# Kernel tuning notes

Hardware: AMD Instinct MI355X
Metric: run time of the kernel (lower is better)

The kernel has to match this reference:

```python
import jax, jax.numpy as jnp
import numpy as np

N_HEAD = 16
D_MODEL = 1024
D_K = 64
D_V = 64
LN_EPS = 1e-6


def setup_inputs() -> dict:
    key = jax.random.key(0)
    ks = jax.random.split(key, 10)
    B, S = 2, 2048
    scale = 0.02
    return {
        "q": jax.random.normal(ks[0], (B, S, D_MODEL), jnp.float32),
        "k": jax.random.normal(ks[1], (B, S, D_MODEL), jnp.float32),
        "v": jax.random.normal(ks[2], (B, S, D_MODEL), jnp.float32),
        "Wq": jax.random.normal(ks[3], (D_MODEL, N_HEAD * D_K), jnp.float32) * scale,
        "Wk": jax.random.normal(ks[4], (D_MODEL, N_HEAD * D_K), jnp.float32) * scale,
        "Wv": jax.random.normal(ks[5], (D_MODEL, N_HEAD * D_V), jnp.float32) * scale,
        "Wfc": jax.random.normal(ks[6], (N_HEAD * D_V, D_MODEL), jnp.float32) * scale,
        "bfc": jnp.zeros((D_MODEL,), jnp.float32),
        "gamma": jnp.ones((D_MODEL,), jnp.float32),
        "beta": jnp.zeros((D_MODEL,), jnp.float32),
    }


def reference(q, k, v, Wq, Wk, Wv, Wfc, bfc, gamma, beta):
    B, S, _ = q.shape
    residual = q
    # QKV projections, split into heads: [B, S, H, Dh]
    qh = (q @ Wq).reshape(B, S, N_HEAD, D_K)
    kh = (k @ Wk).reshape(B, S, N_HEAD, D_K)
    vh = (v @ Wv).reshape(B, S, N_HEAD, D_V)
    # scaled dot-product attention (explicit score matrix, as in source)
    temperature = jnp.asarray(D_K, qh.dtype) ** 0.5
    attn = jnp.einsum("bqhd,bkhd->bhqk", qh, kh) / temperature
    attn = jax.nn.softmax(attn, axis=-1)
    out = jnp.einsum("bhqk,bkhd->bqhd", attn, vh).reshape(B, S, N_HEAD * D_V)
    # output projection (dropout is identity in eval mode)
    out = out @ Wfc + bfc
    # residual + layernorm (eps=1e-6)
    x = out + residual
    mu = jnp.mean(x, axis=-1, keepdims=True)
    var = jnp.mean(jnp.square(x - mu), axis=-1, keepdims=True)
    return (x - mu) / jnp.sqrt(var + LN_EPS) * gamma + beta
```

## Files before the change

kernel.cpp:

```cpp
#include <hip/hip_runtime.h>

typedef float f32x4 __attribute__((ext_vector_type(4)));
typedef short short8 __attribute__((ext_vector_type(8)));
typedef short short4v __attribute__((ext_vector_type(4)));
typedef unsigned short ushort_t;

#define D_MODEL 1024
#define N_HEAD 16
#define SEQ 2048
#define BATCH 2
#define M_TOK 4096
#define HD 1024
#define NT 32
#define APANEL 131072
#define WPANEL 32768
#define QSCALE_L2E 0.1803368801111f

__device__ __forceinline__ ushort_t f2bf(float f) {
    union { float f; unsigned int u; } x; x.f = f;
    unsigned int r = x.u + 0x7fffu + ((x.u >> 16) & 1u);
    return (ushort_t)(r >> 16);
}
__device__ __forceinline__ ushort_t f2bf_fast(float f) {
    union { float f; unsigned int u; } x; x.f = f;
    return (ushort_t)((x.u + 0x8000u) >> 16);
}

__device__ __forceinline__ void async_copy16(const ushort_t* gptr, ushort_t* lptr) {
    __builtin_amdgcn_global_load_lds(
        (const __attribute__((address_space(1))) unsigned int*)gptr,
        (__attribute__((address_space(3))) unsigned int*)lptr, 16, 0, 0);
}

__global__ __launch_bounds__(256) void prep_fused(const float* __restrict__ w0,
                                                  const float* __restrict__ w1,
                                                  const float* __restrict__ w2,
                                                  const float* __restrict__ w3,
                                                  ushort_t* __restrict__ o0,
                                                  ushort_t* __restrict__ o1,
                                                  ushort_t* __restrict__ o2,
                                                  ushort_t* __restrict__ o3,
                                                  const float* __restrict__ q,
                                                  const float* __restrict__ k,
                                                  const float* __restrict__ v,
                                                  ushort_t* __restrict__ qo,
                                                  ushort_t* __restrict__ ko,
                                                  ushort_t* __restrict__ vo) {
    const int z = blockIdx.z;
    const int tid = threadIdx.x;
    const int flat = blockIdx.x + 64 * blockIdx.y;
    if (z < 4) {
        if (flat >= 1024) return;
        const int C = D_MODEL;
        const float* in = (z == 0) ? w0 : (z == 1) ? w1 : (z == 2) ? w2 : w3;
        ushort_t* out = (z == 0) ? o0 : (z == 1) ? o1 : (z == 2) ? o2 : o3;
        __shared__ ushort_t t[32][33];
        int bc = (flat & 31) * 32, br = (flat >> 5) * 32;
        int tx = tid & 31, ty = tid >> 5;
        for (int i = ty; i < 32; i += 8)
            t[i][tx] = f2bf(in[(size_t)(br + i) * C + bc + tx]);
        __syncthreads();
        size_t pbase = (size_t)(br >> 5) * WPANEL;
        for (int i = ty; i < 32; i += 8)
            out[pbase + (size_t)(bc + i) * 32 + tx] = t[tx][i];
    } else {
        const float* s = (z == 4) ? q : (z == 5) ? k : v;
        ushort_t* d = (z == 4) ? qo : (z == 5) ? ko : vo;
        size_t i = ((size_t)flat * 256 + tid) * 8;
        int m = (int)(i >> 10), k0 = (int)(i & 1023);
        float4 a = *(const float4*)(s + i);
        float4 b = *(const float4*)(s + i + 4);
        ushort_t tmp[8] = {f2bf(a.x), f2bf(a.y), f2bf(a.z), f2bf(a.w),
                           f2bf(b.x), f2bf(b.y), f2bf(b.z), f2bf(b.w)};
        *(short8*)(d + (size_t)(k0 >> 5) * APANEL + (size_t)m * 32 + (k0 & 31)) = *(short8*)tmp;
    }
}

__global__ __launch_bounds__(256) void gemm_qkv(const ushort_t* __restrict__ qb,
                                                const ushort_t* __restrict__ kb,
                                                const ushort_t* __restrict__ vb,
                                                const ushort_t* __restrict__ wq,
                                                const ushort_t* __restrict__ wk,
                                                const ushort_t* __restrict__ wv,
                                                ushort_t* __restrict__ Qo,
                                                ushort_t* __restrict__ Ko,
                                                ushort_t* __restrict__ V4) {
    __shared__ ushort_t As[2][128 * 32];
    __shared__ ushort_t Bs[2][128 * 32];
    const int z = blockIdx.z;
    const ushort_t* A = (z == 0) ? qb : (z == 1) ? kb : vb;
    const ushort_t* Bt = (z == 0) ? wq : (z == 1) ? wk : wv;
    const int tid = threadIdx.x;
    const int wave = tid >> 6, lane = tid & 63;
    const int quad = lane >> 4, l16 = lane & 15;
    const int m0 = blockIdx.y * 128, n0 = blockIdx.x * 128;
    const int wm = (wave >> 1) * 64, wn = (wave & 1) * 64;
    const int N = D_MODEL;

    f32x4 acc[4][4];
    for (int i = 0; i < 4; ++i)
        for (int j = 0; j < 4; ++j) acc[i][j] = (f32x4){0.f, 0.f, 0.f, 0.f};

    for (int it = 0; it < 16; ++it) {
        __syncthreads();
        const ushort_t* Ap = A + (size_t)(it * 2) * APANEL + (size_t)m0 * 32;
        const ushort_t* Bp = Bt + (size_t)(it * 2) * WPANEL + (size_t)n0 * 32;
        #pragma unroll
        for (int hf = 0; hf < 2; ++hf) {
            #pragma unroll
            for (int c = 0; c < 2; ++c) {
                int off = (wave * 2 + c) * 512;
                async_copy16(Ap + hf * APANEL + off + lane * 8, &As[hf][off] + lane * 8);
                async_copy16(Bp + hf * WPANEL + off + lane * 8, &Bs[hf][off] + lane * 8);
            }
        }
        __syncthreads();
        short8 af[4][2], bfr[4][2];
        #pragma unroll
        for (int i = 0; i < 4; ++i)
            #pragma unroll
            for (int sk = 0; sk < 2; ++sk)
                af[i][sk] = *(const short8*)&As[sk][(wm + i * 16 + l16) * 32 + quad * 8];
        #pragma unroll
        for (int j = 0; j < 4; ++j)
            #pragma unroll
            for (int sk = 0; sk < 2; ++sk)
                bfr[j][sk] = *(const short8*)&Bs[sk][(wn + j * 16 + l16) * 32 + quad * 8];
        #pragma unroll
        for (int sk = 0; sk < 2; ++sk)
            #pragma unroll
            for (int i = 0; i < 4; ++i)
                #pragma unroll
                for (int j = 0; j < 4; ++j)
                    acc[i][j] = __builtin_amdgcn_mfma_f32_16x16x32_bf16(af[i][sk], bfr[j][sk], acc[i][j], 0, 0, 0);
    }
    if (z == 2) {
        const int tile64 = m0 + wm;
        const int b2 = tile64 >> 11;
        const int kt = (tile64 & 2047) >> 6;
        #pragma unroll
        for (int i = 0; i < 4; ++i)
            #pragma unroll
            for (int j = 0; j < 4; ++j) {
                int n = n0 + wn + j * 16 + l16;
                int h2 = n >> 6, d = n & 63;
                int quadR = (quad + ((n >> 2) & 3)) & 3;
                ushort_t tmp[4];
                #pragma unroll
                for (int r = 0; r < 4; ++r) tmp[r] = f2bf(acc[i][j][r]);
                size_t dst = ((((size_t)(h2 * 2 + b2) * NT + kt) * 4 + i) << 10) + d * 16 + quadR * 4;
                *(short4v*)&V4[dst] = *(short4v*)tmp;
            }
    } else {
        ushort_t* C = (z == 0) ? Qo : Ko;
        const float scale = (z == 0) ? QSCALE_L2E : 1.0f;
        #pragma unroll
        for (int i = 0; i < 4; ++i)
            #pragma unroll
            for (int j = 0; j < 4; ++j) {
                int n = n0 + wn + j * 16 + l16;
                #pragma unroll
                for (int r = 0; r < 4; ++r) {
                    int m = m0 + wm + i * 16 + quad * 4 + r;
                    C[(size_t)m * N + n] = f2bf(acc[i][j][r] * scale);
                }
            }
    }
}

__global__ __launch_bounds__(256) void gemm_fc(const ushort_t* __restrict__ A,
                                               const ushort_t* __restrict__ Bt,
                                               float* __restrict__ Cf,
                                               const float* __restrict__ bias,
                                               const float* __restrict__ resid) {
    __shared__ ushort_t As[2][128 * 32];
    __shared__ ushort_t Bs[2][64 * 32];
    const int tid = threadIdx.x;
    const int wave = tid >> 6, lane = tid & 63;
    const int quad = lane >> 4, l16 = lane & 15;
    const int m0 = blockIdx.y * 128, n0 = blockIdx.x * 64;
    const int N = D_MODEL;

    f32x4 acc[2][4];
    for (int i = 0; i < 2; ++i)
        for (int j = 0; j < 4; ++j) acc[i][j] = (f32x4){0.f, 0.f, 0.f, 0.f};

    for (int it = 0; it < 16; ++it) {
        __syncthreads();
        const ushort_t* Ap = A + (size_t)(it * 2) * APANEL + (size_t)m0 * 32;
        const ushort_t* Bp = Bt + (size_t)(it * 2) * WPANEL + (size_t)n0 * 32;
        #pragma unroll
        for (int c = 0; c < 4; ++c) {
            int g = wave * 4 + c;
            int sk = g >> 3, off = (g & 7) * 512;
            async_copy16(Ap + sk * APANEL + off + lane * 8, &As[sk][off] + lane * 8);
        }
        #pragma unroll
        for (int c = 0; c < 2; ++c) {
            int g = wave * 2 + c;
            int sk = g >> 2, off = (g & 3) * 512;
            async_copy16(Bp + sk * WPANEL + off + lane * 8, &Bs[sk][off] + lane * 8);
        }
        __syncthreads();
        short8 af[2][2], bfr[4][2];
        #pragma unroll
        for (int i = 0; i < 2; ++i)
            #pragma unroll
            for (int sk = 0; sk < 2; ++sk)
                af[i][sk] = *(const short8*)&As[sk][(wave * 32 + i * 16 + l16) * 32 + quad * 8];
        #pragma unroll
        for (int j = 0; j < 4; ++j)
            #pragma unroll
            for (int sk = 0; sk < 2; ++sk)
                bfr[j][sk] = *(const short8*)&Bs[sk][(j * 16 + l16) * 32 + quad * 8];
        #pragma unroll
        for (int sk = 0; sk < 2; ++sk)
            #pragma unroll
            for (int i = 0; i < 2; ++i)
                #pragma unroll
                for (int j = 0; j < 4; ++j)
                    acc[i][j] = __builtin_amdgcn_mfma_f32_16x16x32_bf16(af[i][sk], bfr[j][sk], acc[i][j], 0, 0, 0);
    }
    #pragma unroll
    for (int i = 0; i < 2; ++i)
        #pragma unroll
        for (int j = 0; j < 4; ++j) {
            int n = n0 + j * 16 + l16;
            #pragma unroll
            for (int r = 0; r < 4; ++r) {
                int m = m0 + wave * 32 + i * 16 + quad * 4 + r;
                Cf[(size_t)m * N + n] = acc[i][j][r] + bias[n] + resid[(size_t)m * N + n];
            }
        }
}

__global__ __launch_bounds__(256, 3) void attn64(const ushort_t* __restrict__ Qh,
                                                 const ushort_t* __restrict__ Kh,
                                                 const ushort_t* __restrict__ V4,
                                                 ushort_t* __restrict__ O) {
    __shared__ __align__(16) char smem[25600];
    const int tid = threadIdx.x;
    const int wave = tid >> 6, lane = tid & 63;
    const int quad = lane >> 4, l16 = lane & 15;
    const int h = blockIdx.x, b = blockIdx.y, qt = blockIdx.z;
    const size_t base = (size_t)b * SEQ * HD + h * 64;
    const ushort_t* Qb = Qh + base + (size_t)(qt * 64) * HD;
    const ushort_t* Kb = Kh + base;
    const ushort_t* Vg = V4 + (((size_t)(h * 2 + b) * NT * 4) + wave) * 1024 + lane * 8;

    ushort_t* Vw = (ushort_t*)smem + wave * 3072;
    float* lsb = (float*)(smem + 24576);

    short8 qf[4][2];
    #pragma unroll
    for (int nt = 0; nt < 4; ++nt)
        #pragma unroll
        for (int s = 0; s < 2; ++s)
            qf[nt][s] = *(const short8*)(Qb + (size_t)(nt * 16 + l16) * HD + s * 32 + quad * 8);

    f32x4 oacc[4][4];
    #pragma unroll
    for (int nt = 0; nt < 4; ++nt)
        #pragma unroll
        for (int dt = 0; dt < 4; ++dt) oacc[nt][dt] = (f32x4){0.f, 0.f, 0.f, 0.f};
    float lsum[4] = {0.f, 0.f, 0.f, 0.f};

    const ushort_t* Kr = Kb + (size_t)(wave * 16 + l16) * HD + quad * 8;
    ushort_t* VLd = Vw + lane * 8;

    short8 kf0[2], kf1[2];
    #pragma unroll
    for (int s = 0; s < 2; ++s) kf0[s] = *(const short8*)(Kr + s * 32);
    #pragma unroll
    for (int c = 0; c < 2; ++c) async_copy16(Vg + c * 512, VLd + c * 512);
    #pragma unroll
    for (int c = 0; c < 2; ++c) async_copy16(Vg + 4096 + c * 512, VLd + 1024 + c * 512);

    ushort_t *vb0 = Vw, *vb1 = Vw + 1024, *vb2 = Vw + 2048;
    const int rot = (l16 >> 2) & 3;

    for (int kt = 0; kt < NT; ++kt) {
        if (kt == NT - 1) __builtin_amdgcn_s_waitcnt(0x0F70);
        else              __builtin_amdgcn_s_waitcnt(0x0F72);

        if (kt + 1 < NT) {
            #pragma unroll
            for (int s = 0; s < 2; ++s)
                kf1[s] = *(const short8*)(Kr + (size_t)(kt + 1) * 64 * HD + s * 32);
        }
        if (kt + 2 < NT) {
            #pragma unroll
            for (int c = 0; c < 2; ++c)
                async_copy16(Vg + (size_t)(kt + 2) * 4096 + c * 512, vb2 + lane * 8 + c * 512);
        }

        short4v vf[4];
        #pragma unroll
        for (int dt = 0; dt < 4; ++dt)
            vf[dt] = *(const short4v*)&vb0[(dt * 16 + l16) * 16 + (((quad + rot) & 3) * 4)];

        f32x4 sacc[4];
        #pragma unroll
        for (int nt = 0; nt < 4; ++nt) sacc[nt] = (f32x4){0.f, 0.f, 0.f, 0.f};
        #pragma unroll
        for (int s = 0; s < 2; ++s)
            #pragma unroll
            for (int nt = 0; nt < 4; ++nt)
                sacc[nt] = __builtin_amdgcn_mfma_f32_16x16x32_bf16(kf0[s], qf[nt][s], sacc[nt], 0, 0, 0);

        short4v pf[4];
        #pragma unroll
        for (int nt = 0; nt < 4; ++nt) {
            ushort_t tmp[4];
            #pragma unroll
            for (int i = 0; i < 4; ++i) {
                float pv = __builtin_amdgcn_exp2f(sacc[nt][i]);
                lsum[nt] += pv;
                tmp[i] = f2bf_fast(pv);
            }
            pf[nt] = *(short4v*)tmp;
        }
        #pragma unroll
        for (int nt = 0; nt < 4; ++nt)
            #pragma unroll
            for (int dt = 0; dt < 4; ++dt)
                oacc[nt][dt] = __builtin_amdgcn_mfma_f32_16x16x16bf16_1k(pf[nt], vf[dt], oacc[nt][dt], 0, 0, 0);

        kf0[0] = kf1[0]; kf0[1] = kf1[1];
        ushort_t* t = vb0; vb0 = vb1; vb1 = vb2; vb2 = t;
    }

    #pragma unroll
    for (int nt = 0; nt < 4; ++nt) {
        lsum[nt] += __shfl_xor(lsum[nt], 16, 64);
        lsum[nt] += __shfl_xor(lsum[nt], 32, 64);
    }
    if (quad == 0) {
        #pragma unroll
        for (int nt = 0; nt < 4; ++nt) lsb[wave * 64 + nt * 16 + l16] = lsum[nt];
    }
    __syncthreads();

    float* R = (float*)smem;
    #pragma unroll
    for (int w = 0; w < 4; ++w) {
        if (wave == w) {
            #pragma unroll
            for (int nt = 0; nt < 4; ++nt)
                #pragma unroll
                for (int dt = 0; dt < 4; ++dt)
                    #pragma unroll
                    for (int i = 0; i < 4; ++i) {
                        int idx = (nt * 16 + quad * 4 + i) * 66 + dt * 16 + l16;
                        if (w == 0) R[idx] = oacc[nt][dt][i];
                        else        R[idx] += oacc[nt][dt][i];
                    }
        }
        __syncthreads();
    }
    float inv[4];
    #pragma unroll
    for (int i = 0; i < 4; ++i) {
        int qrow = wave * 16 + quad * 4 + i;
        float t = lsb[qrow] + lsb[64 + qrow] + lsb[128 + qrow] + lsb[192 + qrow];
        inv[i] = 1.f / t;
    }
    #pragma unroll
    for (int i = 0; i < 4; ++i) {
        int qrow = wave * 16 + quad * 4 + i;
        size_t tok = (size_t)b * SEQ + qt * 64 + qrow;
        #pragma unroll
        for (int dt = 0; dt < 4; ++dt) {
            int d = dt * 16 + l16;
            size_t dst = (size_t)(h * 2 + (dt >> 1)) * APANEL + tok * 32 + (dt & 1) * 16 + l16;
            O[dst] = f2bf(R[qrow * 66 + d] * inv[i]);
        }
    }
}

__global__ __launch_bounds__(256) void ln_kernel(float* __restrict__ x,
                                                 const float* __restrict__ gamma,
                                                 const float* __restrict__ beta) {
    const int D = D_MODEL;
    float* xr = x + (size_t)blockIdx.x * D;
    const int tid = threadIdx.x;
    float4 v = *(const float4*)(xr + tid * 4);
    float s = v.x + v.y + v.z + v.w;
    float s2 = v.x * v.x + v.y * v.y + v.z * v.z + v.w * v.w;
    #pragma unroll
    for (int off = 1; off < 64; off <<= 1) {
        s += __shfl_xor(s, off, 64);
        s2 += __shfl_xor(s2, off, 64);
    }
    __shared__ float ws1[4], ws2[4];
    int wave = tid >> 6, lane = tid & 63;
    if (lane == 0) { ws1[wave] = s; ws2[wave] = s2; }
    __syncthreads();
    s = ws1[0] + ws1[1] + ws1[2] + ws1[3];
    s2 = ws2[0] + ws2[1] + ws2[2] + ws2[3];
    float mean = s * (1.f / D);
    float var = s2 * (1.f / D) - mean * mean;
    float rstd = rsqrtf(var + 1e-6f);
    float4 g = *(const float4*)(gamma + tid * 4);
    float4 bt = *(const float4*)(beta + tid * 4);
    float4 o;
    o.x = (v.x - mean) * rstd * g.x + bt.x;
    o.y = (v.y - mean) * rstd * g.y + bt.y;
    o.z = (v.z - mean) * rstd * g.z + bt.z;
    o.w = (v.w - mean) * rstd * g.w + bt.w;
    *(float4*)(xr + tid * 4) = o;
}

extern "C" void kernel_launch(void* const* d_in, const int* in_sizes, int n_in,
                              void* d_out, int out_size, void* d_ws, size_t ws_size,
                              hipStream_t stream) {
    const float* q = (const float*)d_in[0];
    const float* k = (const float*)d_in[1];
    const float* v = (const float*)d_in[2];
    const float* Wq = (const float*)d_in[3];
    const float* Wk = (const float*)d_in[4];
    const float* Wv = (const float*)d_in[5];
    const float* Wfc = (const float*)d_in[6];
    const float* bfc = (const float*)d_in[7];
    const float* gamma = (const float*)d_in[8];
    const float* beta = (const float*)d_in[9];
    float* out = (float*)d_out;

    char* ws = (char*)d_ws;
    const size_t MB = 1u << 20;
    ushort_t* WqT  = (ushort_t*)(ws + 0 * MB);
    ushort_t* WkT  = (ushort_t*)(ws + 2 * MB);
    ushort_t* WvT  = (ushort_t*)(ws + 4 * MB);
    ushort_t* WfcT = (ushort_t*)(ws + 6 * MB);
    ushort_t* qb   = (ushort_t*)(ws + 8 * MB);
    ushort_t* kb   = (ushort_t*)(ws + 16 * MB);
    ushort_t* vb   = (ushort_t*)(ws + 24 * MB);
    ushort_t* Qh   = (ushort_t*)(ws + 32 * MB);
    ushort_t* Kh   = (ushort_t*)(ws + 40 * MB);
    ushort_t* Vt   = (ushort_t*)(ws + 48 * MB);
    ushort_t* Oh   = (ushort_t*)(ws + 8 * MB);

    const int M = M_TOK, D = D_MODEL;
    prep_fused<<<dim3(64, 32, 7), 256, 0, stream>>>(
        Wq, Wk, Wv, Wfc, WqT, WkT, WvT, WfcT, q, k, v, qb, kb, vb);

    gemm_qkv<<<dim3(D / 128, M / 128, 3), 256, 0, stream>>>(qb, kb, vb, WqT, WkT, WvT, Qh, Kh, Vt);

    attn64<<<dim3(N_HEAD, BATCH, SEQ / 64), 256, 0, stream>>>(Qh, Kh, Vt, Oh);

    gemm_fc<<<dim3(D / 64, M / 128), 256, 0, stream>>>(Oh, WfcT, out, bfc, q);

    ln_kernel<<<M, 256, 0, stream>>>(out, gamma, beta);
}
```

Before: 246.1 us.

## Deepen attention K/V prefetch pipeline with 4-slot V ring and unrolled steps

The attention kernel's V ring buffer in shared memory grows from 3 slots to 4, and K fragments are now prefetched two tiles ahead, alternating between two register sets. The main loop is unrolled by four with compile-time slot indices, and the waitcnt immediates are tuned so each step waits only for the oldest outstanding load. The exp/bf16 conversion now uses the packed v_cvt_pk_bf16_f32 instruction. This is meant to hide more global-load latency and cut per-iteration overhead, at the cost of more LDS per block and more registers, which may reduce occupancy.

```diff
diff --git a/kernel.cpp b/kernel.cpp
--- a/kernel.cpp
+++ b/kernel.cpp
@@ -238,7 +238,7 @@
                                                  const ushort_t* __restrict__ Kh,
                                                  const ushort_t* __restrict__ V4,
                                                  ushort_t* __restrict__ O) {
-    __shared__ __align__(16) char smem[25600];
+    __shared__ __align__(16) char smem[33792];
     const int tid = threadIdx.x;
     const int wave = tid >> 6, lane = tid & 63;
     const int quad = lane >> 4, l16 = lane & 15;
@@ -248,8 +248,8 @@
     const ushort_t* Kb = Kh + base;
     const ushort_t* Vg = V4 + (((size_t)(h * 2 + b) * NT * 4) + wave) * 1024 + lane * 8;
 
-    ushort_t* Vw = (ushort_t*)smem + wave * 3072;
-    float* lsb = (float*)(smem + 24576);
+    ushort_t* Vw = (ushort_t*)smem + wave * 4096;
+    float* lsb = (float*)(smem + 32768);
 
     short8 qf[4][2];
     #pragma unroll
@@ -268,67 +268,84 @@
     const ushort_t* Kr = Kb + (size_t)(wave * 16 + l16) * HD + quad * 8;
     ushort_t* VLd = Vw + lane * 8;
 
-    short8 kf0[2], kf1[2];
-    #pragma unroll
-    for (int s = 0; s < 2; ++s) kf0[s] = *(const short8*)(Kr + s * 32);
-    #pragma unroll
-    for (int c = 0; c < 2; ++c) async_copy16(Vg + c * 512, VLd + c * 512);
-    #pragma unroll
-    for (int c = 0; c < 2; ++c) async_copy16(Vg + 4096 + c * 512, VLd + 1024 + c * 512);
-
-    ushort_t *vb0 = Vw, *vb1 = Vw + 1024, *vb2 = Vw + 2048;
+    short8 kfA[2], kfB[2];
+    #pragma unroll
+    for (int s = 0; s < 2; ++s) kfA[s] = *(const short8*)(Kr + s * 32);
+    #pragma unroll
+    for (int s = 0; s < 2; ++s) kfB[s] = *(const short8*)(Kr + (size_t)64 * HD + s * 32);
+    #pragma unroll
+    for (int t = 0; t < 3; ++t)
+        #pragma unroll
+        for (int c = 0; c < 2; ++c)
+            async_copy16(Vg + (size_t)t * 4096 + c * 512, VLd + t * 1024 + c * 512);
+
     const int rot = (l16 >> 2) & 3;
 
-    for (int kt = 0; kt < NT; ++kt) {
-        if (kt == NT - 1) __builtin_amdgcn_s_waitcnt(0x0F70);
-        else              __builtin_amdgcn_s_waitcnt(0x0F72);
-
-        if (kt + 1 < NT) {
-            #pragma unroll
-            for (int s = 0; s < 2; ++s)
-                kf1[s] = *(const short8*)(Kr + (size_t)(kt + 1) * 64 * HD + s * 32);
-        }
-        if (kt + 2 < NT) {
-            #pragma unroll
-            for (int c = 0; c < 2; ++c)
-                async_copy16(Vg + (size_t)(kt + 2) * 4096 + c * 512, vb2 + lane * 8 + c * 512);
-        }
-
-        short4v vf[4];
-        #pragma unroll
-        for (int dt = 0; dt < 4; ++dt)
-            vf[dt] = *(const short4v*)&vb0[(dt * 16 + l16) * 16 + (((quad + rot) & 3) * 4)];
-
-        f32x4 sacc[4];
-        #pragma unroll
-        for (int nt = 0; nt < 4; ++nt) sacc[nt] = (f32x4){0.f, 0.f, 0.f, 0.f};
-        #pragma unroll
-        for (int s = 0; s < 2; ++s)
-            #pragma unroll
-            for (int nt = 0; nt < 4; ++nt)
-                sacc[nt] = __builtin_amdgcn_mfma_f32_16x16x32_bf16(kf0[s], qf[nt][s], sacc[nt], 0, 0, 0);
-
-        short4v pf[4];
-        #pragma unroll
-        for (int nt = 0; nt < 4; ++nt) {
-            ushort_t tmp[4];
-            #pragma unroll
-            for (int i = 0; i < 4; ++i) {
-                float pv = __builtin_amdgcn_exp2f(sacc[nt][i]);
-                lsum[nt] += pv;
-                tmp[i] = f2bf_fast(pv);
-            }
-            pf[nt] = *(short4v*)tmp;
-        }
-        #pragma unroll
-        for (int nt = 0; nt < 4; ++nt)
-            #pragma unroll
-            for (int dt = 0; dt < 4; ++dt)
-                oacc[nt][dt] = __builtin_amdgcn_mfma_f32_16x16x16bf16_1k(pf[nt], vf[dt], oacc[nt][dt], 0, 0, 0);
-
-        kf0[0] = kf1[0]; kf0[1] = kf1[1];
-        ushort_t* t = vb0; vb0 = vb1; vb1 = vb2; vb2 = t;
-    }
+#define ATTN_STEP(KT, SLOT, KFU, WAITIMM, DO_V, DO_K)                                        \
+    {                                                                                        \
+        __builtin_amdgcn_s_waitcnt(WAITIMM);                                                 \
+        if (DO_V) {                                                                          \
+            _Pragma("unroll")                                                                \
+            for (int c = 0; c < 2; ++c)                                                      \
+                async_copy16(Vg + (size_t)((KT) + 3) * 4096 + c * 512,                       \
+                             VLd + (((SLOT) + 3) & 3) * 1024 + c * 512);                     \
+        }                                                                                    \
+        short4v vf[4];                                                                       \
+        _Pragma("unroll")                                                                    \
+        for (int dt = 0; dt < 4; ++dt)                                                       \
+            vf[dt] = *(const short4v*)&Vw[(SLOT) * 1024 + (dt * 16 + l16) * 16               \
+                                          + (((quad + rot) & 3) * 4)];                       \
+        f32x4 sacc[4];                                                                       \
+        _Pragma("unroll")                                                                    \
+        for (int nt = 0; nt < 4; ++nt) sacc[nt] = (f32x4){0.f, 0.f, 0.f, 0.f};               \
+        _Pragma("unroll")                                                                    \
+        for (int s = 0; s < 2; ++s)                                                          \
+            _Pragma("unroll")                                                                \
+            for (int nt = 0; nt < 4; ++nt)                                                   \
+                sacc[nt] = __builtin_amdgcn_mfma_f32_16x16x32_bf16(KFU[s], qf[nt][s],        \
+                                                                   sacc[nt], 0, 0, 0);       \
+        if (DO_K) {                                                                          \
+            _Pragma("unroll")                                                                \
+            for (int s = 0; s < 2; ++s)                                                      \
+                KFU[s] = *(const short8*)(Kr + (size_t)((KT) + 2) * 64 * HD + s * 32);       \
+        }                                                                                    \
+        short4v pf[4];                                                                       \
+        _Pragma("unroll")                                                                    \
+        for (int nt = 0; nt < 4; ++nt) {                                                     \
+            float p0 = __builtin_amdgcn_exp2f(sacc[nt][0]);                                  \
+            float p1 = __builtin_amdgcn_exp2f(sacc[nt][1]);                                  \
+            float p2 = __builtin_amdgcn_exp2f(sacc[nt][2]);                                  \
+            float p3 = __builtin_amdgcn_exp2f(sacc[nt][3]);                                  \
+            lsum[nt] += (p0 + p1) + (p2 + p3);                                               \
+            union { unsigned int u[2]; short4v s4; } pu;                                     \
+            asm("v_cvt_pk_bf16_f32 %0, %1, %2" : "=v"(pu.u[0]) : "v"(p0), "v"(p1));          \
+            asm("v_cvt_pk_bf16_f32 %0, %1, %2" : "=v"(pu.u[1]) : "v"(p2), "v"(p3));          \
+            pf[nt] = pu.s4;                                                                  \
+        }                                                                                    \
+        _Pragma("unroll")                                                                    \
+        for (int nt = 0; nt < 4; ++nt)                                                       \
+            _Pragma("unroll")                                                                \
+            for (int dt = 0; dt < 4; ++dt)                                                   \
+                oacc[nt][dt] = __builtin_amdgcn_mfma_f32_16x16x16bf16_1k(pf[nt], vf[dt],     \
+                                                                         oacc[nt][dt],       \
+                                                                         0, 0, 0);           \
+    }
+
+    ATTN_STEP(0, 0, kfA, 0x0F70, true, true);
+    ATTN_STEP(1, 1, kfB, 0x0F74, true, true);
+    ATTN_STEP(2, 2, kfA, 0x0F74, true, true);
+    ATTN_STEP(3, 3, kfB, 0x0F74, true, true);
+    for (int kt0 = 4; kt0 < 28; kt0 += 4) {
+        ATTN_STEP(kt0 + 0, 0, kfA, 0x0F74, true, true);
+        ATTN_STEP(kt0 + 1, 1, kfB, 0x0F74, true, true);
+        ATTN_STEP(kt0 + 2, 2, kfA, 0x0F74, true, true);
+        ATTN_STEP(kt0 + 3, 3, kfB, 0x0F74, true, true);
+    }
+    ATTN_STEP(28, 0, kfA, 0x0F74, true, true);
+    ATTN_STEP(29, 1, kfB, 0x0F74, false, true);
+    ATTN_STEP(30, 2, kfA, 0x0F72, false, false);
+    ATTN_STEP(31, 3, kfB, 0x0F70, false, false);
+#undef ATTN_STEP
 
     #pragma unroll
     for (int nt = 0; nt < 4; ++nt) {
```

Result: slower. 349.2 us (+41.9%).
